# Kernel tuning notes

Measured on AMD Instinct MI355X. Metric: run time of the kernel, lower is better.

Reference implementation:

```python
import jax, jax.numpy as jnp
import numpy as np

C = 128  # hidden_dim


def setup_inputs() -> dict:
    key = jax.random.key(0)
    ks = jax.random.split(key, 8)
    B, H, W = 4, 64, 64
    x1 = jax.random.normal(ks[0], (B, C, H, W), dtype=jnp.float32)
    x2 = jax.random.normal(ks[1], (B, C, H, W), dtype=jnp.float32)
    # 1x1 conv == per-pixel linear over channels; store weights as [C_out, C_in]
    s = 1.0 / np.sqrt(C)
    wq = jax.random.uniform(ks[2], (C, C), jnp.float32, -s, s)
    bq = jax.random.uniform(ks[3], (C,), jnp.float32, -s, s)
    wk = jax.random.uniform(ks[4], (C, C), jnp.float32, -s, s)
    bk = jax.random.uniform(ks[5], (C,), jnp.float32, -s, s)
    wv = jax.random.uniform(ks[6], (C, C), jnp.float32, -s, s)
    bv = jax.random.uniform(ks[7], (C,), jnp.float32, -s, s)
    return {"x1": x1, "x2": x2, "wq": wq, "bq": bq, "wk": wk, "bk": bk, "wv": wv, "bv": bv}


def reference(x1, x2, wq, bq, wk, bk, wv, bv):
    B, Cc, H, W = x1.shape
    N = H * W
    # flatten spatial -> tokens: [B, N, C]
    t1 = x1.reshape(B, Cc, N).transpose(0, 2, 1)
    t2 = x2.reshape(B, Cc, N).transpose(0, 2, 1)
    # 1x1 conv projections (per-token linear)
    q = jnp.einsum('bnc,oc->bno', t1, wq) + bq
    k = jnp.einsum('bnc,oc->bno', t2, wk) + bk
    v = jnp.einsum('bnc,oc->bno', t2, wv) + bv
    scale = 1.0 / jnp.sqrt(jnp.asarray(Cc, x1.dtype))
    attn = jax.nn.softmax(jnp.einsum('bqc,bkc->bqk', q, k) * scale, axis=-1)
    out = jnp.einsum('bqk,bkc->bqc', attn, v)  # [B, N, C]
    out = out.transpose(0, 2, 1).reshape(B, Cc, H, W)
    return out + x1
```

## Files before the change

kernel.cpp:

```cpp
#include <hip/hip_runtime.h>
#include <hip/hip_bf16.h>

typedef float  f32x4  __attribute__((ext_vector_type(4)));
typedef float  f32x16 __attribute__((ext_vector_type(16)));
typedef short  s16x8  __attribute__((ext_vector_type(8)));
typedef int    i32x8  __attribute__((ext_vector_type(8)));
typedef unsigned int   u32x2 __attribute__((ext_vector_type(2)));
typedef unsigned int   u32x4 __attribute__((ext_vector_type(4)));

#define B_ 4
#define C_ 128
#define N_ 4096
#define NST 16
#define QSCALE 0.12751744f

typedef __attribute__((address_space(3))) unsigned int       lds_u32;
typedef __attribute__((address_space(1))) const unsigned int glb_u32;

__device__ __forceinline__ unsigned int pkbf(float lo, float hi) {
    union { float f; unsigned int u; } a, b; a.f = lo; b.f = hi;
    return __builtin_amdgcn_perm(b.u + 0x8000u, a.u + 0x8000u, 0x07060302u);
}
__device__ __forceinline__ unsigned int pk_fp8x4(float a, float b, float c, float d) {
    int v = __builtin_amdgcn_cvt_pk_fp8_f32(a, b, 0, false);
    v = __builtin_amdgcn_cvt_pk_fp8_f32(c, d, v, true);
    return (unsigned int)v;
}
__device__ __forceinline__ s16x8 mk_frag(unsigned int a, unsigned int b,
                                         unsigned int c, unsigned int d) {
    union { u32x4 u; s16x8 v; } t; t.u = (u32x4){a, b, c, d}; return t.v;
}
__device__ __forceinline__ f32x16 z16() {
    f32x16 v;
    #pragma unroll
    for (int r = 0; r < 16; r++) v[r] = 0.f;
    return v;
}
__device__ __forceinline__ void cp16(const unsigned char* g, unsigned char* l) {
    __builtin_amdgcn_global_load_lds((glb_u32*)g, (lds_u32*)l, 16, 0, 0);
}
__device__ __forceinline__ i32x8 ld32(const unsigned char* p) {
    union { u32x4 q[2]; i32x8 v; } t;
    t.q[0] = *(const u32x4*)p;
    t.q[1] = *(const u32x4*)(p + 1024);
    return t.v;
}
__device__ __forceinline__ f32x16 mfs(i32x8 a, i32x8 b, f32x16 c) {
    return __builtin_amdgcn_mfma_scale_f32_32x32x64_f8f6f4(
        a, b, c, 0, 0, 0, 0x7F7F7F7Fu, 0, 0x7F7F7F7Fu);
}

__global__ __launch_bounds__(256) void wcvt_kernel(
    const float* __restrict__ wq, const float* __restrict__ wk,
    const float* __restrict__ wv, unsigned short* __restrict__ Wf)
{
    const int gid = blockIdx.x * 256 + threadIdx.x;
    const int l = gid & 63, fid = gid >> 6;
    const int kc = fid & 7, ot = (fid >> 3) & 3, z = fid >> 5;
    const float* w = (z == 0) ? wq : (z == 1 ? wk : wv);
    const int o  = 32 * ot + (l & 31);
    const int c0 = 16 * kc + 8 * (l >> 5);
    const float* src = &w[o * C_ + c0];
    *(u32x4*)&Wf[fid * 512 + l * 8] = (u32x4){
        pkbf(src[0], src[1]), pkbf(src[2], src[3]),
        pkbf(src[4], src[5]), pkbf(src[6], src[7])};
}

__global__ __launch_bounds__(256, 2) void proj_kernel(
    const float* __restrict__ x1, const float* __restrict__ x2,
    const float* __restrict__ bq, const float* __restrict__ bk,
    const float* __restrict__ bv,
    const unsigned short* __restrict__ Wf,
    unsigned char* __restrict__ Qf, unsigned char* __restrict__ Kf,
    unsigned char* __restrict__ Vf)
{
    __shared__ float Xs[2][C_ * 36];
    const int tid = threadIdx.x;
    const int ot  = tid >> 6;
    const int l = tid & 63, lo = l & 31, h = l >> 5;
    const int bid = blockIdx.x;
    const int b = bid & 3, tb = bid >> 2;
    const int n0 = tb * 32;

    {
        const int q = tid & 7, c0 = tid >> 3;
        #pragma unroll
        for (int cc = 0; cc < 4; cc++) {
            const int c = c0 + 32 * cc;
            const size_t gof = ((size_t)b * C_ + c) * N_ + n0 + 4 * q;
            *(f32x4*)&Xs[0][c * 36 + 4 * q] = *(const f32x4*)&x1[gof];
            *(f32x4*)&Xs[1][c * 36 + 4 * q] = *(const f32x4*)&x2[gof];
        }
    }
    __syncthreads();

    auto ldW = [&](int z, int kc) -> s16x8 {
        return *(const s16x8*)&Wf[(((z * 4 + ot) * 8) + kc) * 512 + l * 8];
    };
    auto xfrag = [&](int z, int kc) -> s16x8 {
        const float* p = &Xs[z][(16 * kc + 8 * h) * 36 + lo];
        float f[8];
        #pragma unroll
        for (int i = 0; i < 8; i++) f[i] = p[i * 36];
        return mk_frag(pkbf(f[0], f[1]), pkbf(f[2], f[3]),
                       pkbf(f[4], f[5]), pkbf(f[6], f[7]));
    };

    f32x16 aq = z16(), ak = z16(), av = z16();
    s16x8 wqA = ldW(0, 0), wkA = ldW(1, 0), wvA = ldW(2, 0);
    s16x8 wqB, wkB, wvB;
    #pragma unroll
    for (int kc = 0; kc < 8; kc++) {
        if (kc & 1) {
            if (kc < 7) { wqA = ldW(0, kc + 1); wkA = ldW(1, kc + 1); wvA = ldW(2, kc + 1); }
            s16x8 f1 = xfrag(0, kc), f2 = xfrag(1, kc);
            aq = __builtin_amdgcn_mfma_f32_32x32x16_bf16(wqB, f1, aq, 0, 0, 0);
            ak = __builtin_amdgcn_mfma_f32_32x32x16_bf16(wkB, f2, ak, 0, 0, 0);
            av = __builtin_amdgcn_mfma_f32_32x32x16_bf16(f2, wvB, av, 0, 0, 0);
        } else {
            if (kc < 7) { wqB = ldW(0, kc + 1); wkB = ldW(1, kc + 1); wvB = ldW(2, kc + 1); }
            s16x8 f1 = xfrag(0, kc), f2 = xfrag(1, kc);
            aq = __builtin_amdgcn_mfma_f32_32x32x16_bf16(wqA, f1, aq, 0, 0, 0);
            ak = __builtin_amdgcn_mfma_f32_32x32x16_bf16(wkA, f2, ak, 0, 0, 0);
            av = __builtin_amdgcn_mfma_f32_32x32x16_bf16(f2, wvA, av, 0, 0, 0);
        }
    }

    const size_t fbase = (size_t)(b * 128 + tb) * 4096;
    #pragma unroll
    for (int rq = 0; rq < 4; rq++) {
        const int o0 = 32 * ot + 8 * rq + 4 * h;
        const f32x4 b4q = *(const f32x4*)&bq[o0];
        const f32x4 b4k = *(const f32x4*)&bk[o0];
        const size_t off = fbase + (ot >> 1) * 2048 + (rq >> 1) * 1024
                         + ((ot & 1) * 32 + lo) * 16 + 8 * (rq & 1) + 4 * h;
        *(unsigned int*)&Qf[off] = pk_fp8x4(
            (aq[4*rq+0] + b4q[0]) * QSCALE, (aq[4*rq+1] + b4q[1]) * QSCALE,
            (aq[4*rq+2] + b4q[2]) * QSCALE, (aq[4*rq+3] + b4q[3]) * QSCALE);
        *(unsigned int*)&Kf[off] = pk_fp8x4(
            ak[4*rq+0] + b4k[0], ak[4*rq+1] + b4k[1],
            ak[4*rq+2] + b4k[2], ak[4*rq+3] + b4k[3]);
    }
    {
        const float bvv = bv[32 * ot + lo];
        const size_t vbase = ((size_t)(b * 64 + (tb >> 1)) * 4 + ot) * 2048;
        #pragma unroll
        for (int rq = 0; rq < 4; rq++) {
            const size_t off = vbase + (rq >> 1) * 1024
                             + ((tb & 1) * 32 + lo) * 16 + 8 * (rq & 1) + 4 * h;
            *(unsigned int*)&Vf[off] = pk_fp8x4(
                av[4*rq+0] + bvv, av[4*rq+1] + bvv,
                av[4*rq+2] + bvv, av[4*rq+3] + bvv);
        }
    }
}

__global__ __launch_bounds__(512, 1) void attn_kernel(
    const unsigned char* __restrict__ Qf,
    const unsigned char* __restrict__ Kf,
    const unsigned char* __restrict__ Vf,
    const float* __restrict__ x1,
    float* __restrict__ out)
{
    __shared__ __align__(16) unsigned char smem[2][65536];
    __shared__ float Llds[8][32];

    const int tid = threadIdx.x;
    const int w  = tid >> 6;
    const int qi = w & 1, ps = w >> 1;
    const int l = tid & 63, lo = l & 31, h = l >> 5;
    const int bid = blockIdx.x;
    const int xcd = bid & 7, slot = bid >> 3;
    const int b  = xcd >> 1;
    const int qt = ((xcd & 1) << 5) | slot;
    const int q0 = qt * 64;

    const unsigned char* Kb = Kf + (size_t)b * 524288;
    const unsigned char* Vb = Vf + (size_t)b * 524288;

    i32x8 qb0, qb1;
    {
        const unsigned char* qp = Qf + (size_t)(b * 128 + qt * 2 + qi) * 4096 + l * 16;
        qb0 = ld32(qp);
        qb1 = ld32(qp + 2048);
    }

    f32x16 oacc[4];
    #pragma unroll
    for (int ct = 0; ct < 4; ct++) oacc[ct] = z16();
    float La = 0.f, Lb2 = 0.f;

    auto stage = [&](int t, int buf) {
        const int tp = (t + slot) & 15;
        const unsigned char* Ks = Kb + (size_t)tp * 32768;
        const unsigned char* Vs = Vb + (size_t)tp * 32768;
        unsigned char* db = &smem[buf][0];
        #pragma unroll
        for (int j = 0; j < 4; j++) {
            const int c = w + 8 * j;
            cp16(Ks + c * 1024 + l * 16, db + c * 1024);
            cp16(Vs + c * 1024 + l * 16, db + 32768 + c * 1024);
        }
    };

    auto compute = [&](int t) {
        const unsigned char* db  = &smem[t & 1][0];
        const unsigned char* kt0 = db + (2 * ps) * 4096;
        f32x16 s0 = z16(), s1 = z16();
        {
            i32x8 kf0 = ld32(kt0 + l * 16);
            s0 = mfs(kf0, qb0, s0);
            i32x8 kf1 = ld32(kt0 + 2048 + l * 16);
            s0 = mfs(kf1, qb1, s0);
            i32x8 kf2 = ld32(kt0 + 4096 + l * 16);
            s1 = mfs(kf2, qb0, s1);
            i32x8 kf3 = ld32(kt0 + 6144 + l * 16);
            s1 = mfs(kf3, qb1, s1);
        }
        float e0[16], e1[16];
        #pragma unroll
        for (int r = 0; r < 16; r++) {
            e0[r] = __builtin_amdgcn_exp2f(s0[r]);
            e1[r] = __builtin_amdgcn_exp2f(s1[r]);
        }
        #pragma unroll
        for (int r = 0; r < 8; r++) { La += e0[r] + e1[r]; Lb2 += e0[r+8] + e1[r+8]; }
        union { unsigned int u[8]; i32x8 v; } pb;
        #pragma unroll
        for (int j = 0; j < 4; j++) {
            const unsigned int w0 = pk_fp8x4(e0[4*j], e0[4*j+1], e0[4*j+2], e0[4*j+3]);
            const unsigned int w1 = pk_fp8x4(e1[4*j], e1[4*j+1], e1[4*j+2], e1[4*j+3]);
            u32x2 sw = __builtin_amdgcn_permlane32_swap(w0, w1, false, false);
            pb.u[2*j]   = sw[0];
            pb.u[2*j+1] = sw[1];
        }
        const i32x8 pB = pb.v;
        const unsigned char* vb = db + 32768 + (ps * 4) * 2048;
        #pragma unroll
        for (int ct = 0; ct < 4; ct++) {
            i32x8 vA = ld32(vb + ct * 2048 + l * 16);
            oacc[ct] = mfs(vA, pB, oacc[ct]);
        }
    };

    stage(0, 0);
    stage(1, 1);
    asm volatile("s_waitcnt vmcnt(8)" ::: "memory");
    __builtin_amdgcn_s_barrier();
    __builtin_amdgcn_sched_barrier(0);

    for (int t = 0; t < NST; t++) {
        compute(t);
        __builtin_amdgcn_s_barrier();
        if (t + 2 < NST) {
            stage(t + 2, t & 1);
            asm volatile("s_waitcnt vmcnt(8)" ::: "memory");
        } else {
            asm volatile("s_waitcnt vmcnt(0)" ::: "memory");
        }
        __builtin_amdgcn_s_barrier();
        __builtin_amdgcn_sched_barrier(0);
    }

    const float Lh = La + Lb2;
    const float Lsum = Lh + __shfl_xor(Lh, 32, 64);
    if (l < 32) Llds[w][lo] = Lsum;
    __syncthreads();

    float* Ol = (float*)&smem[0][0];
    for (int g = 0; g < 2; g++) {
        if (qi == g) {
            #pragma unroll
            for (int ct = 0; ct < 4; ct++)
                #pragma unroll
                for (int r = 0; r < 16; r++) {
                    const int c = 32 * ct + (r & 3) + 8 * (r >> 2) + 4 * h;
                    Ol[ps * 4224 + c * 33 + lo] = oacc[ct][r];
                }
        }
        __syncthreads();
        {
            const int c = tid >> 2, qq = tid & 3;
            const size_t gbase = ((size_t)b * C_ + c) * N_ + q0 + g * 32 + qq * 8;
            float v[8];
            #pragma unroll
            for (int j = 0; j < 8; j++) {
                const int q = qq * 8 + j;
                const float ssum = Ol[c * 33 + q]        + Ol[4224  + c * 33 + q]
                                 + Ol[8448 + c * 33 + q] + Ol[12672 + c * 33 + q];
                const float Lq = Llds[g][q] + Llds[2 + g][q]
                               + Llds[4 + g][q] + Llds[6 + g][q];
                v[j] = ssum * __builtin_amdgcn_rcpf(Lq);
            }
            const f32x4 xlo = *(const f32x4*)&x1[gbase];
            const f32x4 xhi = *(const f32x4*)&x1[gbase + 4];
            *(f32x4*)&out[gbase]     = (f32x4){v[0]+xlo[0], v[1]+xlo[1], v[2]+xlo[2], v[3]+xlo[3]};
            *(f32x4*)&out[gbase + 4] = (f32x4){v[4]+xhi[0], v[5]+xhi[1], v[6]+xhi[2], v[7]+xhi[3]};
        }
        __syncthreads();
    }
}

extern "C" void kernel_launch(void* const* d_in, const int* in_sizes, int n_in,
                              void* d_out, int out_size, void* d_ws, size_t ws_size,
                              hipStream_t stream)
{
    const float* x1 = (const float*)d_in[0];
    const float* x2 = (const float*)d_in[1];
    const float* wq = (const float*)d_in[2];
    const float* bq = (const float*)d_in[3];
    const float* wk = (const float*)d_in[4];
    const float* bk = (const float*)d_in[5];
    const float* wv = (const float*)d_in[6];
    const float* bv = (const float*)d_in[7];
    float* out = (float*)d_out;

    unsigned short* Wf = (unsigned short*)d_ws;
    unsigned char* Qf = (unsigned char*)d_ws + 98304;
    unsigned char* Kf = Qf + (size_t)B_ * 128 * 4096;
    unsigned char* Vf = Kf + (size_t)B_ * 128 * 4096;

    wcvt_kernel<<<24, 256, 0, stream>>>(wq, wk, wv, Wf);
    proj_kernel<<<512, 256, 0, stream>>>(x1, x2, bq, bk, bv, Wf, Qf, Kf, Vf);
    attn_kernel<<<256, 512, 0, stream>>>(Qf, Kf, Vf, x1, out);
}
```

Baseline: 45.16 us.

## Load K/V fragments directly from global into registers, drop LDS staging

Replaces the double-buffered LDS staging of K and V tiles, which used global_load_lds and per-iteration barriers, with direct global-to-register loads. K for the next tile is software-prefetched while V for the current tile is loaded. LDS shrinks to the output transpose buffer and launch bounds allow two blocks per CU. Without LDS sharing, the two query waves of each pair load the same K/V data separately, which increases global and L2 traffic. In exchange the loop has no barriers and occupancy can be higher.

```diff
diff --git a/kernel.cpp b/kernel.cpp
--- a/kernel.cpp
+++ b/kernel.cpp
@@ -14,9 +14,6 @@
 #define NST 16
 #define QSCALE 0.12751744f
 
-typedef __attribute__((address_space(3))) unsigned int       lds_u32;
-typedef __attribute__((address_space(1))) const unsigned int glb_u32;
-
 __device__ __forceinline__ unsigned int pkbf(float lo, float hi) {
     union { float f; unsigned int u; } a, b; a.f = lo; b.f = hi;
     return __builtin_amdgcn_perm(b.u + 0x8000u, a.u + 0x8000u, 0x07060302u);
@@ -36,10 +33,7 @@
     for (int r = 0; r < 16; r++) v[r] = 0.f;
     return v;
 }
-__device__ __forceinline__ void cp16(const unsigned char* g, unsigned char* l) {
-    __builtin_amdgcn_global_load_lds((glb_u32*)g, (lds_u32*)l, 16, 0, 0);
-}
-__device__ __forceinline__ i32x8 ld32(const unsigned char* p) {
+__device__ __forceinline__ i32x8 ld32g(const unsigned char* p) {
     union { u32x4 q[2]; i32x8 v; } t;
     t.q[0] = *(const u32x4*)p;
     t.q[1] = *(const u32x4*)(p + 1024);
@@ -155,14 +149,14 @@
     }
 }
 
-__global__ __launch_bounds__(512, 1) void attn_kernel(
+__global__ __launch_bounds__(512, 2) void attn_kernel(
     const unsigned char* __restrict__ Qf,
     const unsigned char* __restrict__ Kf,
     const unsigned char* __restrict__ Vf,
     const float* __restrict__ x1,
     float* __restrict__ out)
 {
-    __shared__ __align__(16) unsigned char smem[2][65536];
+    __shared__ float Ol[4 * 128 * 33];
     __shared__ float Llds[8][32];
 
     const int tid = threadIdx.x;
@@ -175,14 +169,14 @@
     const int qt = ((xcd & 1) << 5) | slot;
     const int q0 = qt * 64;
 
-    const unsigned char* Kb = Kf + (size_t)b * 524288;
-    const unsigned char* Vb = Vf + (size_t)b * 524288;
+    const unsigned char* Kb = Kf + (size_t)b * 524288 + 2 * ps * 4096 + l * 16;
+    const unsigned char* Vb = Vf + (size_t)b * 524288 + ps * 8192 + l * 16;
 
     i32x8 qb0, qb1;
     {
         const unsigned char* qp = Qf + (size_t)(b * 128 + qt * 2 + qi) * 4096 + l * 16;
-        qb0 = ld32(qp);
-        qb1 = ld32(qp + 2048);
+        qb0 = ld32g(qp);
+        qb1 = ld32g(qp + 2048);
     }
 
     f32x16 oacc[4];
@@ -190,33 +184,30 @@
     for (int ct = 0; ct < 4; ct++) oacc[ct] = z16();
     float La = 0.f, Lb2 = 0.f;
 
-    auto stage = [&](int t, int buf) {
+    i32x8 k0, k1, k2, k3;
+    {
+        const unsigned char* Kg = Kb + (size_t)(slot & 15) * 32768;
+        k0 = ld32g(Kg);        k1 = ld32g(Kg + 2048);
+        k2 = ld32g(Kg + 4096); k3 = ld32g(Kg + 6144);
+    }
+
+    #pragma unroll
+    for (int t = 0; t < NST; t++) {
         const int tp = (t + slot) & 15;
-        const unsigned char* Ks = Kb + (size_t)tp * 32768;
-        const unsigned char* Vs = Vb + (size_t)tp * 32768;
-        unsigned char* db = &smem[buf][0];
-        #pragma unroll
-        for (int j = 0; j < 4; j++) {
-            const int c = w + 8 * j;
-            cp16(Ks + c * 1024 + l * 16, db + c * 1024);
-            cp16(Vs + c * 1024 + l * 16, db + 32768 + c * 1024);
-        }
-    };
-
-    auto compute = [&](int t) {
-        const unsigned char* db  = &smem[t & 1][0];
-        const unsigned char* kt0 = db + (2 * ps) * 4096;
+        const unsigned char* Vg = Vb + (size_t)tp * 32768;
+        i32x8 v0 = ld32g(Vg);        i32x8 v1 = ld32g(Vg + 2048);
+        i32x8 v2 = ld32g(Vg + 4096); i32x8 v3 = ld32g(Vg + 6144);
+        i32x8 n0, n1, n2, n3;
+        if (t + 1 < NST) {
+            const unsigned char* Kg = Kb + (size_t)((t + 1 + slot) & 15) * 32768;
+            n0 = ld32g(Kg);        n1 = ld32g(Kg + 2048);
+            n2 = ld32g(Kg + 4096); n3 = ld32g(Kg + 6144);
+        }
         f32x16 s0 = z16(), s1 = z16();
-        {
-            i32x8 kf0 = ld32(kt0 + l * 16);
-            s0 = mfs(kf0, qb0, s0);
-            i32x8 kf1 = ld32(kt0 + 2048 + l * 16);
-            s0 = mfs(kf1, qb1, s0);
-            i32x8 kf2 = ld32(kt0 + 4096 + l * 16);
-            s1 = mfs(kf2, qb0, s1);
-            i32x8 kf3 = ld32(kt0 + 6144 + l * 16);
-            s1 = mfs(kf3, qb1, s1);
-        }
+        s0 = mfs(k0, qb0, s0);
+        s0 = mfs(k1, qb1, s0);
+        s1 = mfs(k2, qb0, s1);
+        s1 = mfs(k3, qb1, s1);
         float e0[16], e1[16];
         #pragma unroll
         for (int r = 0; r < 16; r++) {
@@ -235,31 +226,11 @@
             pb.u[2*j+1] = sw[1];
         }
         const i32x8 pB = pb.v;
-        const unsigned char* vb = db + 32768 + (ps * 4) * 2048;
-        #pragma unroll
-        for (int ct = 0; ct < 4; ct++) {
-            i32x8 vA = ld32(vb + ct * 2048 + l * 16);
-            oacc[ct] = mfs(vA, pB, oacc[ct]);
-        }
-    };
-
-    stage(0, 0);
-    stage(1, 1);
-    asm volatile("s_waitcnt vmcnt(8)" ::: "memory");
-    __builtin_amdgcn_s_barrier();
-    __builtin_amdgcn_sched_barrier(0);
-
-    for (int t = 0; t < NST; t++) {
-        compute(t);
-        __builtin_amdgcn_s_barrier();
-        if (t + 2 < NST) {
-            stage(t + 2, t & 1);
-            asm volatile("s_waitcnt vmcnt(8)" ::: "memory");
-        } else {
-            asm volatile("s_waitcnt vmcnt(0)" ::: "memory");
-        }
-        __builtin_amdgcn_s_barrier();
-        __builtin_amdgcn_sched_barrier(0);
+        oacc[0] = mfs(v0, pB, oacc[0]);
+        oacc[1] = mfs(v1, pB, oacc[1]);
+        oacc[2] = mfs(v2, pB, oacc[2]);
+        oacc[3] = mfs(v3, pB, oacc[3]);
+        k0 = n0; k1 = n1; k2 = n2; k3 = n3;
     }
 
     const float Lh = La + Lb2;
@@ -267,7 +238,6 @@
     if (l < 32) Llds[w][lo] = Lsum;
     __syncthreads();
 
-    float* Ol = (float*)&smem[0][0];
     for (int g = 0; g < 2; g++) {
         if (qi == g) {
             #pragma unroll
```

Result: faster. 42.52 us (-5.9%).
